# Performance work log

Hardware: AMD Instinct MI355X
Metric: run time of the kernel (lower is better)

The kernel has to match this reference:

```python
import jax, jax.numpy as jnp
import numpy as np

N_NODES = 100000
N_RELS = 4
N_EDGES = 200000
D_IN = 256
D_OUT = 256
N_BASES = 2
LN_EPS = 1e-5


def setup_inputs() -> dict:
    key = jax.random.key(0)
    ks = jax.random.split(key, 8)
    x = jax.random.normal(ks[0], (N_NODES, D_IN), dtype=jnp.float32)
    src_idx = jax.random.randint(ks[1], (N_RELS, N_EDGES), 0, N_NODES, dtype=jnp.int32)
    dst_idx = jax.random.randint(ks[2], (N_RELS, N_EDGES), 0, N_NODES, dtype=jnp.int32)
    # WeightBasis: bases [B, in, out], per-relation coefficients [R, B]
    xav = float(np.sqrt(2.0)) * float(np.sqrt(6.0 / (D_IN + D_OUT)))
    bases = jax.random.uniform(ks[3], (N_BASES, D_IN, D_OUT), minval=-xav, maxval=xav, dtype=jnp.float32)
    w_comp = jax.random.normal(ks[4], (N_RELS, N_BASES), dtype=jnp.float32) * 0.5
    loop_weight = jax.random.uniform(ks[5], (D_IN, D_OUT), minval=-xav, maxval=xav, dtype=jnp.float32)
    h_bias = jnp.zeros((D_OUT,), dtype=jnp.float32)
    ln_gamma = jnp.ones((D_OUT,), dtype=jnp.float32)
    ln_beta = jnp.zeros((D_OUT,), dtype=jnp.float32)
    return {"x": x, "src_idx": src_idx, "dst_idx": dst_idx, "bases": bases,
            "w_comp": w_comp, "loop_weight": loop_weight, "h_bias": h_bias,
            "ln_gamma": ln_gamma, "ln_beta": ln_beta}


def reference(x, src_idx, dst_idx, bases, w_comp, loop_weight, h_bias, ln_gamma, ln_beta):
    n = x.shape[0]
    # basis combination -> per-relation weights [R, in, out]
    W = jnp.einsum('rb,bio->rio', w_comp, bases)

    def per_rel(W_r, s, d):
        # GraphConv(norm='right', weight=W_r): aggregate src feats to dst,
        # normalize by in-degree (clamped to 1), then matmul.
        msgs = x[s]                                            # [E, in]
        agg = jax.ops.segment_sum(msgs, d, num_segments=n)     # [N, in]
        deg = jax.ops.segment_sum(jnp.ones(d.shape, x.dtype), d, num_segments=n)
        agg = agg / jnp.maximum(deg, 1.0)[:, None]
        return agg @ W_r                                        # [N, out]

    hs = jax.vmap(per_rel)(W, src_idx, dst_idx).sum(axis=0)    # HeteroGraphConv sum aggregate
    # self-loop + bias
    h = hs + x @ loop_weight + h_bias
    # layer norm
    mu = jnp.mean(h, axis=-1, keepdims=True)
    var = jnp.mean(jnp.square(h - mu), axis=-1, keepdims=True)
    h = (h - mu) * jax.lax.rsqrt(var + LN_EPS) * ln_gamma + ln_beta
    # activation (dropout inactive in eval; NGNN has 0 layers)
    return jax.nn.relu(h)
```

## Files before the change

kernel.cpp:

```cpp
#include <hip/hip_runtime.h>


#define NN 100000
#define NR 4
#define NE 200000
#define KDIM 768
#define CAP 32
#define BM 128

typedef __attribute__((ext_vector_type(8))) short short8;
typedef __attribute__((ext_vector_type(16))) float floatx16;

__device__ __forceinline__ unsigned short f2bf(float f) {
  unsigned u = __float_as_uint(f);
  u += 0x7FFFu + ((u >> 16) & 1u);
  return (unsigned short)(u >> 16);
}

__device__ __forceinline__ void gload16(const unsigned short* g, unsigned short* l) {
  __builtin_amdgcn_global_load_lds(
      (const __attribute__((address_space(1))) unsigned int*)g,
      (__attribute__((address_space(3))) unsigned int*)l, 16, 0, 0);
}

__global__ void prep(const float* __restrict__ x, const float* __restrict__ bases,
                     const float* __restrict__ loop_w, const int* __restrict__ src,
                     const int* __restrict__ dst, unsigned short* __restrict__ A,
                     unsigned short* __restrict__ Bt, int* __restrict__ cnt,
                     int* __restrict__ edgebuf) {
  const int b = blockIdx.x;
  const int tid = threadIdx.x;
  if (b < 25000) {
    int q = b * 256 + tid;
    int row = q >> 6;
    int c4 = (q & 63) << 2;
    const float4 v = *(const float4*)(x + (size_t)row * 256 + c4);
    ushort4 u;
    u.x = f2bf(v.x); u.y = f2bf(v.y); u.z = f2bf(v.z); u.w = f2bf(v.w);
    *(ushort4*)(A + (size_t)row * KDIM + 512 + c4) = u;
  } else if (b < 25768) {
    int i = (b - 25000) * 256 + tid;
    int n = i & 255;
    int k = i >> 8;
    float v;
    if (k < 256)      v = bases[k * 256 + n];
    else if (k < 512) v = bases[65536 + (k - 256) * 256 + n];
    else              v = loop_w[(k - 512) * 256 + n];
    Bt[(size_t)n * KDIM + k] = f2bf(v);
  } else {
    int i = (b - 25768) * 256 + tid;
    int r = i / NE;
    int s = src[i];
    int dd = dst[i];
    int pos = atomicAdd(&cnt[dd], 1);
    if (pos < CAP) edgebuf[dd * CAP + pos] = s | (r << 20);
  }
}

__global__ void agg_edges(const int* __restrict__ edgebuf, const int* __restrict__ cnt,
                          const float* __restrict__ w_comp, unsigned short* __restrict__ A) {
  const int tid = threadIdx.x;
  const int lane = tid & 63;
  const int wave = tid >> 6;
  const int half = lane >> 5;
  const int l31 = lane & 31;
  const int d = blockIdx.x * 8 + wave * 2 + half;

  int cc = cnt[d]; cc = cc < CAP ? cc : CAP;
  int ev = 0;
  if (l31 < cc) ev = edgebuf[d * CAP + l31];
  const int rl = ev >> 20;

  unsigned long long b0 = __ballot((l31 < cc) && rl == 0);
  unsigned long long b1 = __ballot((l31 < cc) && rl == 1);
  unsigned long long b2 = __ballot((l31 < cc) && rl == 2);
  unsigned long long b3 = __ballot((l31 < cc) && rl == 3);
  const int sh = half << 5;
  float i0 = 1.0f / fmaxf((float)__popc((unsigned)(b0 >> sh)), 1.0f);
  float i1 = 1.0f / fmaxf((float)__popc((unsigned)(b1 >> sh)), 1.0f);
  float i2 = 1.0f / fmaxf((float)__popc((unsigned)(b2 >> sh)), 1.0f);
  float i3 = 1.0f / fmaxf((float)__popc((unsigned)(b3 >> sh)), 1.0f);
  float s00 = w_comp[0] * i0, s10 = w_comp[1] * i0;
  float s01 = w_comp[2] * i1, s11 = w_comp[3] * i1;
  float s02 = w_comp[4] * i2, s12 = w_comp[5] * i2;
  float s03 = w_comp[6] * i3, s13 = w_comp[7] * i3;

  float a0[8] = {0.f, 0.f, 0.f, 0.f, 0.f, 0.f, 0.f, 0.f};
  float a1[8] = {0.f, 0.f, 0.f, 0.f, 0.f, 0.f, 0.f, 0.f};
  const unsigned short* Xp = A + 512 + l31 * 8;
  const int selbase = lane & 32;

#define EDGE_W(v, w0, w1)                                            \
  int r_##w0 = (v) >> 20;                                            \
  float w0 = r_##w0 < 2 ? (r_##w0 == 0 ? s00 : s01)                  \
                        : (r_##w0 == 2 ? s02 : s03);                 \
  float w1 = r_##w0 < 2 ? (r_##w0 == 0 ? s10 : s11)                  \
                        : (r_##w0 == 2 ? s12 : s13);

#define ACC8(g, w0, w1)                                              \
  {                                                                  \
    float e0 = __uint_as_float((g).x << 16);                         \
    float e1 = __uint_as_float((g).x & 0xFFFF0000u);                 \
    float e2 = __uint_as_float((g).y << 16);                         \
    float e3 = __uint_as_float((g).y & 0xFFFF0000u);                 \
    float e4 = __uint_as_float((g).z << 16);                         \
    float e5 = __uint_as_float((g).z & 0xFFFF0000u);                 \
    float e6 = __uint_as_float((g).w << 16);                         \
    float e7 = __uint_as_float((g).w & 0xFFFF0000u);                 \
    a0[0] += (w0) * e0; a0[1] += (w0) * e1; a0[2] += (w0) * e2;      \
    a0[3] += (w0) * e3; a0[4] += (w0) * e4; a0[5] += (w0) * e5;      \
    a0[6] += (w0) * e6; a0[7] += (w0) * e7;                          \
    a1[0] += (w1) * e0; a1[1] += (w1) * e1; a1[2] += (w1) * e2;      \
    a1[3] += (w1) * e3; a1[4] += (w1) * e4; a1[5] += (w1) * e5;      \
    a1[6] += (w1) * e6; a1[7] += (w1) * e7;                          \
  }

  int i = 0;
  for (; i + 4 <= cc; i += 4) {
    int v0 = __shfl(ev, selbase + i);
    int v1 = __shfl(ev, selbase + i + 1);
    int v2 = __shfl(ev, selbase + i + 2);
    int v3 = __shfl(ev, selbase + i + 3);
    const uint4 g0 = *(const uint4*)(Xp + (size_t)(v0 & 0xFFFFF) * KDIM);
    const uint4 g1 = *(const uint4*)(Xp + (size_t)(v1 & 0xFFFFF) * KDIM);
    const uint4 g2 = *(const uint4*)(Xp + (size_t)(v2 & 0xFFFFF) * KDIM);
    const uint4 g3 = *(const uint4*)(Xp + (size_t)(v3 & 0xFFFFF) * KDIM);
    { EDGE_W(v0, w0a, w1a) ACC8(g0, w0a, w1a) }
    { EDGE_W(v1, w0b, w1b) ACC8(g1, w0b, w1b) }
    { EDGE_W(v2, w0c, w1c) ACC8(g2, w0c, w1c) }
    { EDGE_W(v3, w0d, w1d) ACC8(g3, w0d, w1d) }
  }
  for (; i < cc; ++i) {
    int v = __shfl(ev, selbase + i);
    const uint4 g = *(const uint4*)(Xp + (size_t)(v & 0xFFFFF) * KDIM);
    EDGE_W(v, w0, w1)
    ACC8(g, w0, w1)
  }

  uint4 o0, o1;
  o0.x = (unsigned)f2bf(a0[0]) | ((unsigned)f2bf(a0[1]) << 16);
  o0.y = (unsigned)f2bf(a0[2]) | ((unsigned)f2bf(a0[3]) << 16);
  o0.z = (unsigned)f2bf(a0[4]) | ((unsigned)f2bf(a0[5]) << 16);
  o0.w = (unsigned)f2bf(a0[6]) | ((unsigned)f2bf(a0[7]) << 16);
  o1.x = (unsigned)f2bf(a1[0]) | ((unsigned)f2bf(a1[1]) << 16);
  o1.y = (unsigned)f2bf(a1[2]) | ((unsigned)f2bf(a1[3]) << 16);
  o1.z = (unsigned)f2bf(a1[4]) | ((unsigned)f2bf(a1[5]) << 16);
  o1.w = (unsigned)f2bf(a1[6]) | ((unsigned)f2bf(a1[7]) << 16);
  *(uint4*)(A + (size_t)d * KDIM + l31 * 8) = o0;
  *(uint4*)(A + (size_t)d * KDIM + 256 + l31 * 8) = o1;
}

__launch_bounds__(256, 2)
__global__ void gemm_ln(const unsigned short* __restrict__ A, const unsigned short* __restrict__ Bt,
                        const float* __restrict__ h_bias, const float* __restrict__ gamma,
                        const float* __restrict__ beta, float* __restrict__ out) {
  __shared__ unsigned short As[4 * 2 * 512];
  __shared__ unsigned short Bs[8 * 2 * 512];
  const int tid = threadIdx.x;
  const int wave = tid >> 6;
  const int lane = tid & 63;
  const int l31 = lane & 31;
  const int half = lane >> 5;
  const int m0 = blockIdx.x * BM;

  floatx16 acc[8];
#pragma unroll
  for (int t = 0; t < 8; ++t)
#pragma unroll
    for (int r = 0; r < 16; ++r) acc[t][r] = 0.0f;

  int arow = m0 + wave * 32 + l31;
  if (arow >= NN) arow = NN - 1;
  const unsigned short* gA = A + (size_t)arow * KDIM + half * 8;
  const unsigned short* gBa = Bt + (size_t)(wave * 64 + l31) * KDIM + half * 8;
  const unsigned short* gBb = gBa + 32 * KDIM;
  unsigned short* lA0 = As + (wave * 2 + 0) * 512 + lane * 8;
  unsigned short* lA1 = As + (wave * 2 + 1) * 512 + lane * 8;
  unsigned short* lB0 = Bs + ((wave * 2 + 0) * 2 + 0) * 512 + lane * 8;
  unsigned short* lB1 = Bs + ((wave * 2 + 0) * 2 + 1) * 512 + lane * 8;
  unsigned short* lB2 = Bs + ((wave * 2 + 1) * 2 + 0) * 512 + lane * 8;
  unsigned short* lB3 = Bs + ((wave * 2 + 1) * 2 + 1) * 512 + lane * 8;

  for (int k0 = 0; k0 < KDIM; k0 += 32) {
    gload16(gA + k0, lA0);
    gload16(gA + k0 + 16, lA1);
    gload16(gBa + k0, lB0);
    gload16(gBa + k0 + 16, lB1);
    gload16(gBb + k0, lB2);
    gload16(gBb + k0 + 16, lB3);
    __syncthreads();
#pragma unroll
    for (int kk = 0; kk < 2; ++kk) {
      short8 af = *(const short8*)(As + (wave * 2 + kk) * 512 + lane * 8);
#pragma unroll
      for (int t = 0; t < 8; ++t) {
        short8 bfr = *(const short8*)(Bs + (t * 2 + kk) * 512 + lane * 8);
        acc[t] = __builtin_amdgcn_mfma_f32_32x32x16_bf16(af, bfr, acc[t], 0, 0, 0);
      }
    }
    __syncthreads();
  }

  float bcol[8], gc[8], bc[8];
#pragma unroll
  for (int t = 0; t < 8; ++t) {
    int col = t * 32 + l31;
    bcol[t] = h_bias[col];
    gc[t] = gamma[col];
    bc[t] = beta[col];
  }
#pragma unroll
  for (int t = 0; t < 8; ++t)
#pragma unroll
    for (int r = 0; r < 16; ++r) acc[t][r] += bcol[t];

  const int m_base = m0 + wave * 32;
#pragma unroll
  for (int r = 0; r < 16; ++r) {
    float s = 0.f, q = 0.f;
#pragma unroll
    for (int t = 0; t < 8; ++t) { float v = acc[t][r]; s += v; q += v * v; }
#pragma unroll
    for (int m = 16; m >= 1; m >>= 1) {
      s += __shfl_xor(s, m);
      q += __shfl_xor(q, m);
    }
    float mean = s * (1.0f / 256.0f);
    float var = q * (1.0f / 256.0f) - mean * mean;
    float rstd = rsqrtf(var + 1e-5f);
    int row = (r & 3) + ((r >> 2) << 3) + (half << 2);
    int grow = m_base + row;
    if (grow < NN) {
#pragma unroll
      for (int t = 0; t < 8; ++t) {
        float v = (acc[t][r] - mean) * rstd * gc[t] + bc[t];
        out[(size_t)grow * 256 + t * 32 + l31] = fmaxf(v, 0.0f);
      }
    }
  }
}

extern "C" void kernel_launch(void* const* d_in, const int* in_sizes, int n_in,
                              void* d_out, int out_size, void* d_ws, size_t ws_size,
                              hipStream_t stream) {
  const float* x      = (const float*)d_in[0];
  const int*   src    = (const int*)d_in[1];
  const int*   dst    = (const int*)d_in[2];
  const float* bases  = (const float*)d_in[3];
  const float* w_comp = (const float*)d_in[4];
  const float* loop_w = (const float*)d_in[5];
  const float* h_bias = (const float*)d_in[6];
  const float* gamma  = (const float*)d_in[7];
  const float* beta   = (const float*)d_in[8];
  float* out = (float*)d_out;

  char* ws = (char*)d_ws;
  unsigned short* A  = (unsigned short*)ws;
  unsigned short* Bt = (unsigned short*)(ws + 153600000);
  int* cnt     = (int*)(ws + 153993216);
  int* edgebuf = (int*)(ws + 154393216);

  hipMemsetAsync(cnt, 0, 400000, stream);

  prep<<<28893, 256, 0, stream>>>(x, bases, loop_w, src, dst, A, Bt, cnt, edgebuf);
  agg_edges<<<12500, 256, 0, stream>>>(edgebuf, cnt, w_comp, A);
  gemm_ln<<<(NN + BM - 1) / BM, 256, 0, stream>>>(A, Bt, h_bias, gamma, beta, out);
}
```

Baseline: 413.4 us.

## Load A fragments directly to registers with double buffering and stage B in larger K chunks

The GEMM no longer stages A through LDS. Each wave loads its A fragments straight from global memory into registers, double-buffered across six K stages of 128. B is staged into a larger 64KB LDS buffer per 128-wide K chunk, which needs fewer barriers than the old 32-wide steps. Separately, the x-to-bf16 conversion in prep now handles 8 elements per thread over 4 iterations, which cuts the block count. The larger LDS footprint and extra registers for A may reduce occupancy, and B loads are not overlapped with compute.

```diff
diff --git a/kernel.cpp b/kernel.cpp
--- a/kernel.cpp
+++ b/kernel.cpp
@@ -30,16 +30,24 @@
                      int* __restrict__ edgebuf) {
   const int b = blockIdx.x;
   const int tid = threadIdx.x;
-  if (b < 25000) {
-    int q = b * 256 + tid;
-    int row = q >> 6;
-    int c4 = (q & 63) << 2;
-    const float4 v = *(const float4*)(x + (size_t)row * 256 + c4);
-    ushort4 u;
-    u.x = f2bf(v.x); u.y = f2bf(v.y); u.z = f2bf(v.z); u.w = f2bf(v.w);
-    *(ushort4*)(A + (size_t)row * KDIM + 512 + c4) = u;
-  } else if (b < 25768) {
-    int i = (b - 25000) * 256 + tid;
+  if (b < 3125) {
+    int base = b * 256 + tid;
+#pragma unroll
+    for (int p = 0; p < 4; ++p) {
+      int c = base + p * 800000;
+      int row = c >> 5;
+      int off = (c & 31) << 3;
+      const float4 v0 = *(const float4*)(x + (size_t)row * 256 + off);
+      const float4 v1 = *(const float4*)(x + (size_t)row * 256 + off + 4);
+      uint4 u;
+      u.x = (unsigned)f2bf(v0.x) | ((unsigned)f2bf(v0.y) << 16);
+      u.y = (unsigned)f2bf(v0.z) | ((unsigned)f2bf(v0.w) << 16);
+      u.z = (unsigned)f2bf(v1.x) | ((unsigned)f2bf(v1.y) << 16);
+      u.w = (unsigned)f2bf(v1.z) | ((unsigned)f2bf(v1.w) << 16);
+      *(uint4*)(A + (size_t)row * KDIM + 512 + off) = u;
+    }
+  } else if (b < 3893) {
+    int i = (b - 3125) * 256 + tid;
     int n = i & 255;
     int k = i >> 8;
     float v;
@@ -48,7 +56,7 @@
     else              v = loop_w[(k - 512) * 256 + n];
     Bt[(size_t)n * KDIM + k] = f2bf(v);
   } else {
-    int i = (b - 25768) * 256 + tid;
+    int i = (b - 3893) * 256 + tid;
     int r = i / NE;
     int s = src[i];
     int dd = dst[i];
@@ -154,8 +162,7 @@
 __global__ void gemm_ln(const unsigned short* __restrict__ A, const unsigned short* __restrict__ Bt,
                         const float* __restrict__ h_bias, const float* __restrict__ gamma,
                         const float* __restrict__ beta, float* __restrict__ out) {
-  __shared__ unsigned short As[4 * 2 * 512];
-  __shared__ unsigned short Bs[8 * 2 * 512];
+  __shared__ unsigned short Bs[64 * 512];
   const int tid = threadIdx.x;
   const int wave = tid >> 6;
   const int lane = tid & 63;
@@ -172,33 +179,47 @@
   int arow = m0 + wave * 32 + l31;
   if (arow >= NN) arow = NN - 1;
   const unsigned short* gA = A + (size_t)arow * KDIM + half * 8;
-  const unsigned short* gBa = Bt + (size_t)(wave * 64 + l31) * KDIM + half * 8;
-  const unsigned short* gBb = gBa + 32 * KDIM;
-  unsigned short* lA0 = As + (wave * 2 + 0) * 512 + lane * 8;
-  unsigned short* lA1 = As + (wave * 2 + 1) * 512 + lane * 8;
-  unsigned short* lB0 = Bs + ((wave * 2 + 0) * 2 + 0) * 512 + lane * 8;
-  unsigned short* lB1 = Bs + ((wave * 2 + 0) * 2 + 1) * 512 + lane * 8;
-  unsigned short* lB2 = Bs + ((wave * 2 + 1) * 2 + 0) * 512 + lane * 8;
-  unsigned short* lB3 = Bs + ((wave * 2 + 1) * 2 + 1) * 512 + lane * 8;
-
-  for (int k0 = 0; k0 < KDIM; k0 += 32) {
-    gload16(gA + k0, lA0);
-    gload16(gA + k0 + 16, lA1);
-    gload16(gBa + k0, lB0);
-    gload16(gBa + k0 + 16, lB1);
-    gload16(gBb + k0, lB2);
-    gload16(gBb + k0 + 16, lB3);
-    __syncthreads();
-#pragma unroll
-    for (int kk = 0; kk < 2; ++kk) {
-      short8 af = *(const short8*)(As + (wave * 2 + kk) * 512 + lane * 8);
+
+#define STAGE_B(s)                                                        \
+  {                                                                       \
+    const int kb = (s) * 128;                                             \
+    _Pragma("unroll")                                                     \
+    for (int q = 0; q < 16; ++q) {                                        \
+      const int t = wave * 2 + (q >> 3);                                  \
+      const int j = q & 7;                                                \
+      gload16(Bt + (size_t)(t * 32 + l31) * KDIM + kb + j * 16 + half * 8,\
+              Bs + (t * 8 + j) * 512 + lane * 8);                         \
+    }                                                                     \
+  }
+
+  short8 ab[2][8];
+#pragma unroll
+  for (int j = 0; j < 8; ++j) ab[0][j] = *(const short8*)(gA + j * 16);
+  STAGE_B(0)
+  __syncthreads();
+
+#pragma unroll
+  for (int s = 0; s < 6; ++s) {
+    const int cur = s & 1;
+    if (s < 5) {
+#pragma unroll
+      for (int j = 0; j < 8; ++j)
+        ab[cur ^ 1][j] = *(const short8*)(gA + (s + 1) * 128 + j * 16);
+    }
+#pragma unroll
+    for (int j = 0; j < 8; ++j) {
+      short8 af = ab[cur][j];
 #pragma unroll
       for (int t = 0; t < 8; ++t) {
-        short8 bfr = *(const short8*)(Bs + (t * 2 + kk) * 512 + lane * 8);
+        short8 bfr = *(const short8*)(Bs + (t * 8 + j) * 512 + lane * 8);
         acc[t] = __builtin_amdgcn_mfma_f32_32x32x16_bf16(af, bfr, acc[t], 0, 0, 0);
       }
     }
-    __syncthreads();
+    if (s < 5) {
+      __syncthreads();
+      STAGE_B(s + 1)
+      __syncthreads();
+    }
   }
 
   float bcol[8], gc[8], bc[8];
@@ -262,7 +283,7 @@
 
   hipMemsetAsync(cnt, 0, 400000, stream);
 
-  prep<<<28893, 256, 0, stream>>>(x, bases, loop_w, src, dst, A, Bt, cnt, edgebuf);
+  prep<<<7018, 256, 0, stream>>>(x, bases, loop_w, src, dst, A, Bt, cnt, edgebuf);
   agg_edges<<<12500, 256, 0, stream>>>(edgebuf, cnt, w_comp, A);
   gemm_ln<<<(NN + BM - 1) / BM, 256, 0, stream>>>(A, Bt, h_bias, gamma, beta, out);
 }
```

New measurement: 417.0 us. No clear change (+0.9%).
